# Optimization experiments

Hardware: AMD Instinct MI355X
Metric: run time of the kernel (lower is better)

Reference implementation:

```python
import jax, jax.numpy as jnp
import numpy as np

B, T, D, H = 64, 512, 512, 512

def setup_inputs() -> dict:
    key = jax.random.key(0)
    k1, k2, k3 = jax.random.split(key, 3)
    s_in = 1.0 / np.sqrt(D)
    s_h = 1.0 / np.sqrt(H)
    return {
        "x": jax.random.normal(k1, (B, T, D), dtype=jnp.float32),
        "Wi": jax.random.normal(k2, (D, 3 * H), dtype=jnp.float32) * s_in,  # packed [ir|iz|in]
        "bi": jnp.zeros((3 * H,), dtype=jnp.float32),
        "Wh": jax.random.normal(k3, (H, 3 * H), dtype=jnp.float32) * s_h,   # packed [hr|hz|hn]
        "bhn": jnp.zeros((H,), dtype=jnp.float32),
    }

def reference(x, Wi, bi, Wh, bhn):
    # Flax GRUCell semantics (sigmoid gates, tanh candidate), single layer,
    # zero initial carry, outputs stacked over time plus final carry.
    Bsz, Tlen, _ = x.shape
    Hdim = Wh.shape[0]
    # Precompute all input projections in one big GEMM: [B,T,3H]
    gi_all = jnp.einsum('btd,dk->btk', x, Wi) + bi

    def step(h, gi):
        hr, hz, hn = jnp.split(h @ Wh, 3, axis=-1)
        ir, iz, in_ = jnp.split(gi, 3, axis=-1)
        r = jax.nn.sigmoid(ir + hr)
        z = jax.nn.sigmoid(iz + hz)
        n = jnp.tanh(in_ + r * (hn + bhn))
        h_new = (1.0 - z) * n + z * h
        return h_new, h_new

    h0 = jnp.zeros((Bsz, Hdim), dtype=x.dtype)
    carry, ys = jax.lax.scan(step, h0, jnp.swapaxes(gi_all, 0, 1))  # scan over time
    outputs = jnp.swapaxes(ys, 0, 1)  # [B,T,H]
    return outputs, carry
```

## Files before the change

kernel.cpp:

```cpp
#include <hip/hip_runtime.h>


#define BSZ 64
#define TLEN 512
#define DDIM 512
#define HDIM 512
#define NGRP 4
#define PBLK 32
#define GB 16
#define SLOTB 16384
#define GRPB 65536
#define SENT32 0x40004000u
#define GUARD (1 << 16)

typedef _Float16 half8 __attribute__((ext_vector_type(8)));
typedef _Float16 half4v __attribute__((ext_vector_type(4)));
typedef float f32x4 __attribute__((ext_vector_type(4)));

__device__ __forceinline__ float sigmf(float v) { return 1.f / (1.f + __expf(-v)); }

__global__ void gru_setup(const float* __restrict__ x, _Float16* __restrict__ xb,
                          unsigned* __restrict__ exch) {
  size_t gid = (size_t)blockIdx.x * blockDim.x + threadIdx.x;
  size_t stride = (size_t)gridDim.x * blockDim.x;
  const float4* x4 = (const float4*)x;
  size_t nx4 = (size_t)BSZ * TLEN * DDIM / 4;
  for (size_t i = gid; i < nx4; i += stride) {
    float4 v = x4[i];
    half4v o = {(_Float16)v.x, (_Float16)v.y, (_Float16)v.z, (_Float16)v.w};
    *(half4v*)(xb + 4 * i) = o;
  }
  for (size_t i = gid; i < (size_t)NGRP * GRPB / 4; i += stride) exch[i] = SENT32;
}

__device__ __forceinline__ unsigned chk16(const half8* ah) {
  unsigned dirty = 0;
#pragma unroll
  for (int kt = 0; kt < 16; ++kt) {
    uint4 c;
    __builtin_memcpy(&c, &ah[kt], 16);
    unsigned bad = ((c.x & 0xFFFFu) == 0x4000u) | ((c.y & 0xFFFFu) == 0x4000u) |
                   ((c.z & 0xFFFFu) == 0x4000u) | ((c.w & 0xFFFFu) == 0x4000u);
    dirty |= bad << kt;
  }
  return dirty;
}

__global__ __launch_bounds__(192, 1) void gru_rec(
    const _Float16* __restrict__ xb, const float* __restrict__ Wi,
    const float* __restrict__ Wh, const float* __restrict__ bi,
    const float* __restrict__ bhn, char* __restrict__ exch,
    float* __restrict__ out) {
  __shared__ _Float16 Wh_l[48 * 512];
  __shared__ _Float16 Wi_l[48 * 512];
  __shared__ _Float16 Ah_l[16 * 512];
  __shared__ float Gh_l[2][3 * 256];
  __shared__ float Gx_l[2][3 * 256];

  const int tid = threadIdx.x;
  const int lane = tid & 63;
  const int wid = tid >> 6;
  const int g = blockIdx.x >> 5;
  const int rank = blockIdx.x & 31;
  const int c0 = rank * 16;
  char* const exg = exch + (size_t)g * GRPB;

  for (int idx = tid; idx < 48 * 512; idx += 192) {
    int k = idx / 48;
    int r = idx - k * 48;
    int gate = r >> 4, j = r & 15;
    int col = gate * 512 + c0 + j;
    int phys = (r << 10) | ((((k >> 3) << 4) ^ ((r & 7) << 4))) | ((k & 7) << 1);
    *(_Float16*)((char*)Wi_l + phys) = (_Float16)Wi[(size_t)k * 1536 + col];
    *(_Float16*)((char*)Wh_l + phys) = (_Float16)Wh[(size_t)k * 1536 + col];
  }

  const int m0 = lane >> 3;
  const int cp = (lane & 7) * 2;
  float bir[2], biz[2], bin_[2], bh2[2];
#pragma unroll
  for (int u = 0; u < 2; ++u) {
    bir[u] = bi[c0 + cp + u];
    biz[u] = bi[512 + c0 + cp + u];
    bin_[u] = bi[1024 + c0 + cp + u];
    bh2[u] = bhn[c0 + cp + u];
  }
  float hreg[2][2] = {{0.f, 0.f}, {0.f, 0.f}};
  __syncthreads();

  const int ar = lane & 15;
  const int kg = lane >> 4;
  const int wrow = wid * 16 + ar;
  const int mbat = g * GB + ar;
  const _Float16* const xrow = xb + (size_t)mbat * (TLEN * DDIM);
  char* const hbase = exg + ((kg >> 1) * 512 + ar * 32 + (kg & 1) * 16);
  const int abase = ar << 10;
  const int axor = (ar & 7) << 4;

  for (int t = 0; t < TLEN; ++t) {
    half8 a_x[16];
    const half8* xs = (const half8*)(xrow + (size_t)t * DDIM);
#pragma unroll
    for (int kt = 0; kt < 16; ++kt) a_x[kt] = xs[kt * 4 + kg];
    f32x4 acc_x = {0.f, 0.f, 0.f, 0.f};
#pragma unroll
    for (int kt = 0; kt < 16; ++kt) {
      const int off = (((kt * 4 + kg) << 4) ^ axor);
      half8 b_i = *(const half8*)((const char*)Wi_l + (wrow << 10) + off);
      acc_x = __builtin_amdgcn_mfma_f32_16x16x32_f16(a_x[kt], b_i, acc_x, 0, 0, 0);
    }

    if (wid == 2) {
      unsigned* rst = (unsigned*)(exg + ((t + 2) & 3) * SLOTB + rank * 512);
      __hip_atomic_store(rst + lane, SENT32, __ATOMIC_RELAXED, __HIP_MEMORY_SCOPE_AGENT);
      __hip_atomic_store(rst + 64 + lane, SENT32, __ATOMIC_RELAXED,
                         __HIP_MEMORY_SCOPE_AGENT);
    }
    if (wid == 1 && t > 0) {
      char* hb = hbase + (t & 3) * SLOTB;
      const char* p0 = hb;
      const char* p1 = hb + 4096;
      const char* p2 = hb + 8192;
      const char* p3 = hb + 12288;
      half8 ah[16];
      unsigned dirty;
      int guard = 0;
      do {
        asm volatile(
            "global_load_dwordx4 %0,  %16, off sc1\n\t"
            "global_load_dwordx4 %1,  %16, off offset:1024 sc1\n\t"
            "global_load_dwordx4 %2,  %16, off offset:2048 sc1\n\t"
            "global_load_dwordx4 %3,  %16, off offset:3072 sc1\n\t"
            "global_load_dwordx4 %4,  %17, off sc1\n\t"
            "global_load_dwordx4 %5,  %17, off offset:1024 sc1\n\t"
            "global_load_dwordx4 %6,  %17, off offset:2048 sc1\n\t"
            "global_load_dwordx4 %7,  %17, off offset:3072 sc1\n\t"
            "global_load_dwordx4 %8,  %18, off sc1\n\t"
            "global_load_dwordx4 %9,  %18, off offset:1024 sc1\n\t"
            "global_load_dwordx4 %10, %18, off offset:2048 sc1\n\t"
            "global_load_dwordx4 %11, %18, off offset:3072 sc1\n\t"
            "global_load_dwordx4 %12, %19, off sc1\n\t"
            "global_load_dwordx4 %13, %19, off offset:1024 sc1\n\t"
            "global_load_dwordx4 %14, %19, off offset:2048 sc1\n\t"
            "global_load_dwordx4 %15, %19, off offset:3072 sc1\n\t"
            "s_waitcnt vmcnt(0)"
            : "=&v"(ah[0]), "=&v"(ah[1]), "=&v"(ah[2]), "=&v"(ah[3]),
              "=&v"(ah[4]), "=&v"(ah[5]), "=&v"(ah[6]), "=&v"(ah[7]),
              "=&v"(ah[8]), "=&v"(ah[9]), "=&v"(ah[10]), "=&v"(ah[11]),
              "=&v"(ah[12]), "=&v"(ah[13]), "=&v"(ah[14]), "=&v"(ah[15])
            : "v"(p0), "v"(p1), "v"(p2), "v"(p3));
        dirty = chk16(ah);
      } while (__any(dirty != 0u) && ++guard < GUARD);
#pragma unroll
      for (int kt = 0; kt < 16; ++kt) {
        *(half8*)((char*)Ah_l + (abase | ((kt * 64 + kg * 16) ^ axor))) = ah[kt];
      }
    }
    __syncthreads();

    f32x4 acc_h = {0.f, 0.f, 0.f, 0.f};
    if (t > 0) {
#pragma unroll
      for (int kt = 0; kt < 16; ++kt) {
        half8 a_h = *(const half8*)((const char*)Ah_l +
                                    (abase | ((kt * 64 + kg * 16) ^ axor)));
        const int off = (((kt * 4 + kg) << 4) ^ axor);
        half8 b_h = *(const half8*)((const char*)Wh_l + (wrow << 10) + off);
        acc_h = __builtin_amdgcn_mfma_f32_16x16x32_f16(a_h, b_h, acc_h, 0, 0, 0);
      }
    }
#pragma unroll
    for (int q = 0; q < 4; ++q) {
      int row = kg * 4 + q;
      Gh_l[t & 1][wid * 256 + row * 16 + ar] = acc_h[q];
      Gx_l[t & 1][wid * 256 + row * 16 + ar] = acc_x[q];
    }
    __syncthreads();

    if (wid == 0) {
      const float* GhT = Gh_l[t & 1];
      const float* GxT = Gx_l[t & 1];
      char* pub = exg + ((t + 1) & 3) * SLOTB + rank * 512;
      float hn2[2][2];
#pragma unroll
      for (int bsel = 0; bsel < 2; ++bsel) {
        const int m = m0 + 8 * bsel;
#pragma unroll
        for (int u = 0; u < 2; ++u) {
          const int gi_ = m * 16 + cp + u;
          float r = sigmf(GxT[gi_] + GhT[gi_] + bir[u]);
          float z = sigmf(GxT[256 + gi_] + GhT[256 + gi_] + biz[u]);
          float pren = GxT[512 + gi_] + bin_[u] + r * (GhT[512 + gi_] + bh2[u]);
          float n = 2.f / (1.f + __expf(-2.f * pren)) - 1.f;
          hn2[bsel][u] = (1.f - z) * n + z * hreg[bsel][u];
          hreg[bsel][u] = hn2[bsel][u];
        }
        _Float16 q0 = (_Float16)hn2[bsel][0], q1 = (_Float16)hn2[bsel][1];
        unsigned pu = ((unsigned)*(unsigned short*)&q1 << 16) | *(unsigned short*)&q0;
        __hip_atomic_store((unsigned*)(pub + m * 32 + cp * 2), pu, __ATOMIC_RELAXED,
                           __HIP_MEMORY_SCOPE_AGENT);
      }
#pragma unroll
      for (int bsel = 0; bsel < 2; ++bsel) {
        const int b = g * GB + m0 + 8 * bsel;
        *(float2*)(out + ((size_t)b * TLEN + t) * HDIM + c0 + cp) =
            make_float2(hn2[bsel][0], hn2[bsel][1]);
      }
    }
  }

  if (wid == 0) {
#pragma unroll
    for (int bsel = 0; bsel < 2; ++bsel) {
      const int b = g * GB + m0 + 8 * bsel;
      *(float2*)(out + (size_t)BSZ * TLEN * HDIM + (size_t)b * HDIM + c0 + cp) =
          make_float2(hreg[bsel][0], hreg[bsel][1]);
    }
  }
}

extern "C" void kernel_launch(void* const* d_in, const int* in_sizes, int n_in,
                              void* d_out, int out_size, void* d_ws, size_t ws_size,
                              hipStream_t stream) {
  const float* x = (const float*)d_in[0];
  const float* Wi = (const float*)d_in[1];
  const float* bi = (const float*)d_in[2];
  const float* Wh = (const float*)d_in[3];
  const float* bhn = (const float*)d_in[4];
  float* out = (float*)d_out;

  char* ws = (char*)d_ws;
  _Float16* xb = (_Float16*)ws;
  char* exch = ws + 33554432;

  gru_setup<<<4096, 256, 0, stream>>>(x, xb, (unsigned*)exch);
  gru_rec<<<NGRP * PBLK, 192, 0, stream>>>(xb, Wi, Wh, bi, bhn, exch, out);
}
```

Measured before the change: 1.713 ms.

## Use row-major h exchange layout and issue h poll loads before input GEMM

Changes the global hidden-state exchange buffer to a batch-row-major layout, so each lane reads one contiguous 256-byte chunk instead of four strided pointers. The first poll of the recurrent state is issued at the top of the timestep, before the x-projection MFMAs, so its latency overlaps that compute; the spin loop only reloads when sentinel values remain. The publish and sentinel-reset addressing and the LDS store pattern are rewritten to match. This adds register pressure from holding the 16 prefetched vectors across the input GEMM.

```diff
diff --git a/kernel.cpp b/kernel.cpp
--- a/kernel.cpp
+++ b/kernel.cpp
@@ -11,6 +11,7 @@
 #define SLOTB 16384
 #define GRPB 65536
 #define SENT32 0x40004000u
+#define SENT64 0x4000400040004000ull
 #define GUARD (1 << 16)
 
 typedef _Float16 half8 __attribute__((ext_vector_type(8)));
@@ -93,11 +94,41 @@
   const int wrow = wid * 16 + ar;
   const int mbat = g * GB + ar;
   const _Float16* const xrow = xb + (size_t)mbat * (TLEN * DDIM);
-  char* const hbase = exg + ((kg >> 1) * 512 + ar * 32 + (kg & 1) * 16);
+  const int pb = lane >> 2;
+  const int pq = lane & 3;
+  const int sbase = pb << 10;
+  const int sxor = (pb & 7) << 4;
   const int abase = ar << 10;
   const int axor = (ar & 7) << 4;
 
   for (int t = 0; t < TLEN; ++t) {
+    half8 ah[16];
+    const char* pp = exg + (t & 3) * SLOTB + lane * 256;
+    if (wid == 1 && t > 0) {
+      asm volatile(
+          "global_load_dwordx4 %0,  %16, off sc1\n\t"
+          "global_load_dwordx4 %1,  %16, off offset:16 sc1\n\t"
+          "global_load_dwordx4 %2,  %16, off offset:32 sc1\n\t"
+          "global_load_dwordx4 %3,  %16, off offset:48 sc1\n\t"
+          "global_load_dwordx4 %4,  %16, off offset:64 sc1\n\t"
+          "global_load_dwordx4 %5,  %16, off offset:80 sc1\n\t"
+          "global_load_dwordx4 %6,  %16, off offset:96 sc1\n\t"
+          "global_load_dwordx4 %7,  %16, off offset:112 sc1\n\t"
+          "global_load_dwordx4 %8,  %16, off offset:128 sc1\n\t"
+          "global_load_dwordx4 %9,  %16, off offset:144 sc1\n\t"
+          "global_load_dwordx4 %10, %16, off offset:160 sc1\n\t"
+          "global_load_dwordx4 %11, %16, off offset:176 sc1\n\t"
+          "global_load_dwordx4 %12, %16, off offset:192 sc1\n\t"
+          "global_load_dwordx4 %13, %16, off offset:208 sc1\n\t"
+          "global_load_dwordx4 %14, %16, off offset:224 sc1\n\t"
+          "global_load_dwordx4 %15, %16, off offset:240 sc1"
+          : "=&v"(ah[0]), "=&v"(ah[1]), "=&v"(ah[2]), "=&v"(ah[3]),
+            "=&v"(ah[4]), "=&v"(ah[5]), "=&v"(ah[6]), "=&v"(ah[7]),
+            "=&v"(ah[8]), "=&v"(ah[9]), "=&v"(ah[10]), "=&v"(ah[11]),
+            "=&v"(ah[12]), "=&v"(ah[13]), "=&v"(ah[14]), "=&v"(ah[15])
+          : "v"(pp));
+    }
+
     half8 a_x[16];
     const half8* xs = (const half8*)(xrow + (size_t)t * DDIM);
 #pragma unroll
@@ -111,49 +142,46 @@
     }
 
     if (wid == 2) {
-      unsigned* rst = (unsigned*)(exg + ((t + 2) & 3) * SLOTB + rank * 512);
-      __hip_atomic_store(rst + lane, SENT32, __ATOMIC_RELAXED, __HIP_MEMORY_SCOPE_AGENT);
-      __hip_atomic_store(rst + 64 + lane, SENT32, __ATOMIC_RELAXED,
-                         __HIP_MEMORY_SCOPE_AGENT);
-    }
+      char* rst = exg + ((t + 2) & 3) * SLOTB;
+      __hip_atomic_store(
+          (unsigned long long*)(rst + pb * 1024 + c0 * 2 + pq * 8), SENT64,
+          __ATOMIC_RELAXED, __HIP_MEMORY_SCOPE_AGENT);
+    }
+
     if (wid == 1 && t > 0) {
-      char* hb = hbase + (t & 3) * SLOTB;
-      const char* p0 = hb;
-      const char* p1 = hb + 4096;
-      const char* p2 = hb + 8192;
-      const char* p3 = hb + 12288;
-      half8 ah[16];
-      unsigned dirty;
+      asm volatile("s_waitcnt vmcnt(0)" ::: "memory");
+      __builtin_amdgcn_sched_barrier(0);
+      unsigned dirty = chk16(ah);
       int guard = 0;
-      do {
+      while (__any(dirty != 0u) && ++guard < GUARD) {
         asm volatile(
             "global_load_dwordx4 %0,  %16, off sc1\n\t"
-            "global_load_dwordx4 %1,  %16, off offset:1024 sc1\n\t"
-            "global_load_dwordx4 %2,  %16, off offset:2048 sc1\n\t"
-            "global_load_dwordx4 %3,  %16, off offset:3072 sc1\n\t"
-            "global_load_dwordx4 %4,  %17, off sc1\n\t"
-            "global_load_dwordx4 %5,  %17, off offset:1024 sc1\n\t"
-            "global_load_dwordx4 %6,  %17, off offset:2048 sc1\n\t"
-            "global_load_dwordx4 %7,  %17, off offset:3072 sc1\n\t"
-            "global_load_dwordx4 %8,  %18, off sc1\n\t"
-            "global_load_dwordx4 %9,  %18, off offset:1024 sc1\n\t"
-            "global_load_dwordx4 %10, %18, off offset:2048 sc1\n\t"
-            "global_load_dwordx4 %11, %18, off offset:3072 sc1\n\t"
-            "global_load_dwordx4 %12, %19, off sc1\n\t"
-            "global_load_dwordx4 %13, %19, off offset:1024 sc1\n\t"
-            "global_load_dwordx4 %14, %19, off offset:2048 sc1\n\t"
-            "global_load_dwordx4 %15, %19, off offset:3072 sc1\n\t"
+            "global_load_dwordx4 %1,  %16, off offset:16 sc1\n\t"
+            "global_load_dwordx4 %2,  %16, off offset:32 sc1\n\t"
+            "global_load_dwordx4 %3,  %16, off offset:48 sc1\n\t"
+            "global_load_dwordx4 %4,  %16, off offset:64 sc1\n\t"
+            "global_load_dwordx4 %5,  %16, off offset:80 sc1\n\t"
+            "global_load_dwordx4 %6,  %16, off offset:96 sc1\n\t"
+            "global_load_dwordx4 %7,  %16, off offset:112 sc1\n\t"
+            "global_load_dwordx4 %8,  %16, off offset:128 sc1\n\t"
+            "global_load_dwordx4 %9,  %16, off offset:144 sc1\n\t"
+            "global_load_dwordx4 %10, %16, off offset:160 sc1\n\t"
+            "global_load_dwordx4 %11, %16, off offset:176 sc1\n\t"
+            "global_load_dwordx4 %12, %16, off offset:192 sc1\n\t"
+            "global_load_dwordx4 %13, %16, off offset:208 sc1\n\t"
+            "global_load_dwordx4 %14, %16, off offset:224 sc1\n\t"
+            "global_load_dwordx4 %15, %16, off offset:240 sc1\n\t"
             "s_waitcnt vmcnt(0)"
             : "=&v"(ah[0]), "=&v"(ah[1]), "=&v"(ah[2]), "=&v"(ah[3]),
               "=&v"(ah[4]), "=&v"(ah[5]), "=&v"(ah[6]), "=&v"(ah[7]),
               "=&v"(ah[8]), "=&v"(ah[9]), "=&v"(ah[10]), "=&v"(ah[11]),
               "=&v"(ah[12]), "=&v"(ah[13]), "=&v"(ah[14]), "=&v"(ah[15])
-            : "v"(p0), "v"(p1), "v"(p2), "v"(p3));
+            : "v"(pp));
         dirty = chk16(ah);
-      } while (__any(dirty != 0u) && ++guard < GUARD);
-#pragma unroll
-      for (int kt = 0; kt < 16; ++kt) {
-        *(half8*)((char*)Ah_l + (abase | ((kt * 64 + kg * 16) ^ axor))) = ah[kt];
+      }
+#pragma unroll
+      for (int c = 0; c < 16; ++c) {
+        *(half8*)((char*)Ah_l + (sbase | ((pq * 256 + c * 16) ^ sxor))) = ah[c];
       }
     }
     __syncthreads();
@@ -180,7 +208,7 @@
     if (wid == 0) {
       const float* GhT = Gh_l[t & 1];
       const float* GxT = Gx_l[t & 1];
-      char* pub = exg + ((t + 1) & 3) * SLOTB + rank * 512;
+      char* pub = exg + ((t + 1) & 3) * SLOTB;
       float hn2[2][2];
 #pragma unroll
       for (int bsel = 0; bsel < 2; ++bsel) {
@@ -197,8 +225,8 @@
         }
         _Float16 q0 = (_Float16)hn2[bsel][0], q1 = (_Float16)hn2[bsel][1];
         unsigned pu = ((unsigned)*(unsigned short*)&q1 << 16) | *(unsigned short*)&q0;
-        __hip_atomic_store((unsigned*)(pub + m * 32 + cp * 2), pu, __ATOMIC_RELAXED,
-                           __HIP_MEMORY_SCOPE_AGENT);
+        __hip_atomic_store((unsigned*)(pub + m * 1024 + (c0 + cp) * 2), pu,
+                           __ATOMIC_RELAXED, __HIP_MEMORY_SCOPE_AGENT);
       }
 #pragma unroll
       for (int bsel = 0; bsel < 2; ++bsel) {
```

Result: slower. 3.009 ms (+75.6%).

## Hoist input projection into separate parallel GEMM and halve recurrent block count

Applied to the files above, without the earlier changes.

Adds a standalone MFMA GEMM kernel that computes all input projections plus bias into an fp16 workspace before the recurrence, instead of computing x·Wi inside every timestep of the serial loop. The recurrent kernel now uses 16 blocks per group with 32 columns each and 6 waves, so only the h·Wh product stays on the critical path and fewer blocks take part in each step's exchange. This removes per-step x loads and Wi MFMAs from the latency-bound loop, at the cost of a large fp16 gi buffer (about 100MB) and extra memory traffic. It falls back to the old path if the workspace is too small.

```diff
diff --git a/kernel.cpp b/kernel.cpp
--- a/kernel.cpp
+++ b/kernel.cpp
@@ -5,12 +5,8 @@
 #define TLEN 512
 #define DDIM 512
 #define HDIM 512
-#define NGRP 4
-#define PBLK 32
-#define GB 16
-#define SLOTB 16384
-#define GRPB 65536
 #define SENT32 0x40004000u
+#define SENT64 0x4000400040004000ull
 #define GUARD (1 << 16)
 
 typedef _Float16 half8 __attribute__((ext_vector_type(8)));
@@ -18,6 +14,257 @@
 typedef float f32x4 __attribute__((ext_vector_type(4)));
 
 __device__ __forceinline__ float sigmf(float v) { return 1.f / (1.f + __expf(-v)); }
+__device__ __forceinline__ float lo16(unsigned u) {
+  unsigned short s = (unsigned short)(u & 0xffffu);
+  _Float16 f;
+  __builtin_memcpy(&f, &s, 2);
+  return (float)f;
+}
+__device__ __forceinline__ float hi16(unsigned u) {
+  unsigned short s = (unsigned short)(u >> 16);
+  _Float16 f;
+  __builtin_memcpy(&f, &s, 2);
+  return (float)f;
+}
+
+__device__ __forceinline__ unsigned chk16(const half8* ah) {
+  unsigned dirty = 0;
+#pragma unroll
+  for (int kt = 0; kt < 16; ++kt) {
+    uint4 c;
+    __builtin_memcpy(&c, &ah[kt], 16);
+    unsigned bad = ((c.x & 0xFFFFu) == 0x4000u) | ((c.y & 0xFFFFu) == 0x4000u) |
+                   ((c.z & 0xFFFFu) == 0x4000u) | ((c.w & 0xFFFFu) == 0x4000u);
+    dirty |= bad << kt;
+  }
+  return dirty;
+}
+
+#define SWEEP16(AH, P0, P1, P2, P3)                                           \
+  asm volatile(                                                               \
+      "global_load_dwordx4 %0,  %16, off sc1\n\t"                             \
+      "global_load_dwordx4 %1,  %16, off offset:1024 sc1\n\t"                 \
+      "global_load_dwordx4 %2,  %16, off offset:2048 sc1\n\t"                 \
+      "global_load_dwordx4 %3,  %16, off offset:3072 sc1\n\t"                 \
+      "global_load_dwordx4 %4,  %17, off sc1\n\t"                             \
+      "global_load_dwordx4 %5,  %17, off offset:1024 sc1\n\t"                 \
+      "global_load_dwordx4 %6,  %17, off offset:2048 sc1\n\t"                 \
+      "global_load_dwordx4 %7,  %17, off offset:3072 sc1\n\t"                 \
+      "global_load_dwordx4 %8,  %18, off sc1\n\t"                             \
+      "global_load_dwordx4 %9,  %18, off offset:1024 sc1\n\t"                 \
+      "global_load_dwordx4 %10, %18, off offset:2048 sc1\n\t"                 \
+      "global_load_dwordx4 %11, %18, off offset:3072 sc1\n\t"                 \
+      "global_load_dwordx4 %12, %19, off sc1\n\t"                             \
+      "global_load_dwordx4 %13, %19, off offset:1024 sc1\n\t"                 \
+      "global_load_dwordx4 %14, %19, off offset:2048 sc1\n\t"                 \
+      "global_load_dwordx4 %15, %19, off offset:3072 sc1\n\t"                 \
+      "s_waitcnt vmcnt(0)"                                                    \
+      : "=&v"(AH[0]), "=&v"(AH[1]), "=&v"(AH[2]), "=&v"(AH[3]), "=&v"(AH[4]), \
+        "=&v"(AH[5]), "=&v"(AH[6]), "=&v"(AH[7]), "=&v"(AH[8]), "=&v"(AH[9]), \
+        "=&v"(AH[10]), "=&v"(AH[11]), "=&v"(AH[12]), "=&v"(AH[13]),           \
+        "=&v"(AH[14]), "=&v"(AH[15])                                          \
+      : "v"(P0), "v"(P1), "v"(P2), "v"(P3))
+
+
+__global__ void setup_fast(unsigned* __restrict__ exch) {
+  size_t gid = (size_t)blockIdx.x * blockDim.x + threadIdx.x;
+  size_t stride = (size_t)gridDim.x * blockDim.x;
+  for (size_t i = gid; i < 65536; i += stride) exch[i] = SENT32;
+}
+
+__global__ __launch_bounds__(384, 1) void gemm_gi(const float* __restrict__ x,
+                                                  const float* __restrict__ Wi,
+                                                  const float* __restrict__ bi,
+                                                  _Float16* __restrict__ gi) {
+  __shared__ _Float16 W_l[96 * 512];
+  __shared__ _Float16 A_l[16 * 512];
+  __shared__ _Float16 O_l[16 * 96];
+
+  const int tid = threadIdx.x;
+  const int lane = tid & 63;
+  const int wid = tid >> 6;
+  const int cb = blockIdx.x & 15;
+  const int mp = blockIdx.x >> 4;
+  const int n0 = cb * 96;
+
+  for (int idx = tid; idx < 96 * 512; idx += 384) {
+    int k = idx / 96;
+    int r = idx - k * 96;
+    int phys = (r << 10) | ((((k >> 3) << 4) ^ ((r & 7) << 4))) | ((k & 7) << 1);
+    *(_Float16*)((char*)W_l + phys) = (_Float16)Wi[(size_t)k * 1536 + n0 + r];
+  }
+  const int ar = lane & 15;
+  const int kg = lane >> 4;
+  const int wrow = wid * 16 + ar;
+  const int axor = (ar & 7) << 4;
+  const float bin = bi[n0 + wid * 16 + ar];
+  __syncthreads();
+
+  const float4* x4 = (const float4*)x;
+  for (int mc = 0; mc < 64; ++mc) {
+    const int m0 = (mp * 64 + mc) * 16;
+    for (int i = tid; i < 2048; i += 384) {
+      int r = i >> 7, kq = i & 127, k = kq * 4;
+      float4 v = x4[(size_t)(m0 + r) * 128 + kq];
+      half4v o = {(_Float16)v.x, (_Float16)v.y, (_Float16)v.z, (_Float16)v.w};
+      int phys = (r << 10) | ((((k >> 3) << 4) ^ ((r & 7) << 4))) | ((k & 7) << 1);
+      *(half4v*)((char*)A_l + phys) = o;
+    }
+    __syncthreads();
+    f32x4 acc = {0.f, 0.f, 0.f, 0.f};
+#pragma unroll
+    for (int kt = 0; kt < 16; ++kt) {
+      const int off = (((kt * 4 + kg) << 4) ^ axor);
+      half8 a = *(const half8*)((const char*)A_l + (ar << 10) + off);
+      half8 b = *(const half8*)((const char*)W_l + (wrow << 10) + off);
+      acc = __builtin_amdgcn_mfma_f32_16x16x32_f16(a, b, acc, 0, 0, 0);
+    }
+#pragma unroll
+    for (int q = 0; q < 4; ++q)
+      O_l[(kg * 4 + q) * 96 + wid * 16 + ar] = (_Float16)(acc[q] + bin);
+    __syncthreads();
+    {
+      int row = tid / 24, seg = tid % 24;
+      if (row < 16) {
+        *(unsigned long long*)(gi + (size_t)(m0 + row) * 1536 + n0 + seg * 4) =
+            ((const unsigned long long*)O_l)[row * 24 + seg];
+      }
+    }
+    __syncthreads();
+  }
+}
+
+__global__ __launch_bounds__(384, 1) void gru_rec16(
+    const _Float16* __restrict__ gi, const float* __restrict__ Wh,
+    const float* __restrict__ bhn, char* __restrict__ exch,
+    float* __restrict__ out) {
+  __shared__ _Float16 Wh_l[96 * 512];
+  __shared__ _Float16 Ah_l[16 * 512];
+  __shared__ float Gh_l[2][6 * 256];
+
+  const int tid = threadIdx.x;
+  const int lane = tid & 63;
+  const int wid = tid >> 6;
+  const int g = blockIdx.x >> 4;
+  const int rank = blockIdx.x & 15;
+  const int c0 = rank * 32;
+  char* const exg = exch + (size_t)g * 65536;
+
+  for (int idx = tid; idx < 96 * 512; idx += 384) {
+    int k = idx / 96;
+    int r = idx - k * 96;
+    int col = (r >> 5) * 512 + c0 + (r & 31);
+    int phys = (r << 10) | ((((k >> 3) << 4) ^ ((r & 7) << 4))) | ((k & 7) << 1);
+    *(_Float16*)((char*)Wh_l + phys) = (_Float16)Wh[(size_t)k * 1536 + col];
+  }
+
+  const int e0 = ((wid & 3) * 64 + lane) * 2;
+  const int m = e0 >> 5;
+  const int c = e0 & 31;
+  const int bglob = g * 16 + m;
+  const _Float16* const giR =
+      gi + (size_t)bglob * TLEN * 1536 + c0 + c;
+  const _Float16* const giZ = giR + 512;
+  const _Float16* const giN = giR + 1024;
+  float bh2[2];
+  bh2[0] = bhn[c0 + c];
+  bh2[1] = bhn[c0 + c + 1];
+  float hreg[2] = {0.f, 0.f};
+  __syncthreads();
+
+  const int ar = lane & 15;
+  const int kg = lane >> 4;
+  const int wrow = wid * 16 + ar;
+  const int axor = (ar & 7) << 4;
+  const int abase = ar << 10;
+  char* const hbase = exg + ar * 64 + kg * 16;
+
+  for (int t = 0; t < TLEN; ++t) {
+    if (wid == 4) {
+      unsigned long long* rst = (unsigned long long*)(exg + ((t + 2) & 3) * 16384 +
+                                                      rank * 1024 + lane * 16);
+      __hip_atomic_store(rst, SENT64, __ATOMIC_RELAXED, __HIP_MEMORY_SCOPE_AGENT);
+      __hip_atomic_store(rst + 1, SENT64, __ATOMIC_RELAXED, __HIP_MEMORY_SCOPE_AGENT);
+    }
+    unsigned ur = 0, uz = 0, un = 0;
+    if (wid < 4) {
+      const size_t toff = (size_t)t * 1536;
+      ur = *(const unsigned*)(giR + toff);
+      uz = *(const unsigned*)(giZ + toff);
+      un = *(const unsigned*)(giN + toff);
+    }
+    if (wid == 5 && t > 0) {
+      char* hb = hbase + (t & 3) * 16384;
+      const char* p0 = hb;
+      const char* p1 = hb + 4096;
+      const char* p2 = hb + 8192;
+      const char* p3 = hb + 12288;
+      half8 ah[16];
+      unsigned dirty;
+      int guard = 0;
+      do {
+        SWEEP16(ah, p0, p1, p2, p3);
+        dirty = chk16(ah);
+      } while (__any(dirty != 0u) && ++guard < GUARD);
+#pragma unroll
+      for (int kt = 0; kt < 16; ++kt) {
+        *(half8*)((char*)Ah_l + (abase | ((kt * 64 + kg * 16) ^ axor))) = ah[kt];
+      }
+    }
+    __syncthreads();
+
+    f32x4 acc_h = {0.f, 0.f, 0.f, 0.f};
+    if (t > 0) {
+#pragma unroll
+      for (int kt = 0; kt < 16; ++kt) {
+        half8 a_h = *(const half8*)((const char*)Ah_l +
+                                    (abase | ((kt * 64 + kg * 16) ^ axor)));
+        const int off = (((kt * 4 + kg) << 4) ^ axor);
+        half8 b_h = *(const half8*)((const char*)Wh_l + (wrow << 10) + off);
+        acc_h = __builtin_amdgcn_mfma_f32_16x16x32_f16(a_h, b_h, acc_h, 0, 0, 0);
+      }
+    }
+#pragma unroll
+    for (int q = 0; q < 4; ++q)
+      Gh_l[t & 1][wid * 256 + (kg * 4 + q) * 16 + ar] = acc_h[q];
+    __syncthreads();
+
+    if (wid < 4) {
+      const float* GhT = Gh_l[t & 1];
+      const int ti = (c >> 4);
+      const int cc = c & 15;
+      float hn2[2];
+      const float gir[2] = {lo16(ur), hi16(ur)};
+      const float giz[2] = {lo16(uz), hi16(uz)};
+      const float gin[2] = {lo16(un), hi16(un)};
+#pragma unroll
+      for (int u = 0; u < 2; ++u) {
+        const int gidx = m * 16 + cc + u;
+        float hr = GhT[(0 * 2 + ti) * 256 + gidx];
+        float hz = GhT[(1 * 2 + ti) * 256 + gidx];
+        float hn = GhT[(2 * 2 + ti) * 256 + gidx];
+        float r = sigmf(gir[u] + hr);
+        float z = sigmf(giz[u] + hz);
+        float pren = gin[u] + r * (hn + bh2[u]);
+        float n = 2.f / (1.f + __expf(-2.f * pren)) - 1.f;
+        hn2[u] = (1.f - z) * n + z * hreg[u];
+        hreg[u] = hn2[u];
+      }
+      _Float16 q0 = (_Float16)hn2[0], q1 = (_Float16)hn2[1];
+      unsigned pu = ((unsigned)*(unsigned short*)&q1 << 16) | *(unsigned short*)&q0;
+      __hip_atomic_store(
+          (unsigned*)(exg + ((t + 1) & 3) * 16384 + rank * 1024 + m * 64 + c * 2),
+          pu, __ATOMIC_RELAXED, __HIP_MEMORY_SCOPE_AGENT);
+      *(float2*)(out + ((size_t)bglob * TLEN + t) * HDIM + c0 + c) =
+          make_float2(hn2[0], hn2[1]);
+    }
+  }
+  if (wid < 4) {
+    *(float2*)(out + (size_t)BSZ * TLEN * HDIM + (size_t)bglob * HDIM + c0 + c) =
+        make_float2(hreg[0], hreg[1]);
+  }
+}
+
 
 __global__ void gru_setup(const float* __restrict__ x, _Float16* __restrict__ xb,
                           unsigned* __restrict__ exch) {
@@ -30,20 +277,7 @@
     half4v o = {(_Float16)v.x, (_Float16)v.y, (_Float16)v.z, (_Float16)v.w};
     *(half4v*)(xb + 4 * i) = o;
   }
-  for (size_t i = gid; i < (size_t)NGRP * GRPB / 4; i += stride) exch[i] = SENT32;
-}
-
-__device__ __forceinline__ unsigned chk16(const half8* ah) {
-  unsigned dirty = 0;
-#pragma unroll
-  for (int kt = 0; kt < 16; ++kt) {
-    uint4 c;
-    __builtin_memcpy(&c, &ah[kt], 16);
-    unsigned bad = ((c.x & 0xFFFFu) == 0x4000u) | ((c.y & 0xFFFFu) == 0x4000u) |
-                   ((c.z & 0xFFFFu) == 0x4000u) | ((c.w & 0xFFFFu) == 0x4000u);
-    dirty |= bad << kt;
-  }
-  return dirty;
+  for (size_t i = gid; i < 65536; i += stride) exch[i] = SENT32;
 }
 
 __global__ __launch_bounds__(192, 1) void gru_rec(
@@ -63,7 +297,7 @@
   const int g = blockIdx.x >> 5;
   const int rank = blockIdx.x & 31;
   const int c0 = rank * 16;
-  char* const exg = exch + (size_t)g * GRPB;
+  char* const exg = exch + (size_t)g * 65536;
 
   for (int idx = tid; idx < 48 * 512; idx += 192) {
     int k = idx / 48;
@@ -74,7 +308,6 @@
     *(_Float16*)((char*)Wi_l + phys) = (_Float16)Wi[(size_t)k * 1536 + col];
     *(_Float16*)((char*)Wh_l + phys) = (_Float16)Wh[(size_t)k * 1536 + col];
   }
-
   const int m0 = lane >> 3;
   const int cp = (lane & 7) * 2;
   float bir[2], biz[2], bin_[2], bh2[2];
@@ -91,13 +324,18 @@
   const int ar = lane & 15;
   const int kg = lane >> 4;
   const int wrow = wid * 16 + ar;
-  const int mbat = g * GB + ar;
-  const _Float16* const xrow = xb + (size_t)mbat * (TLEN * DDIM);
+  const int axor = (ar & 7) << 4;
+  const int abase = ar << 10;
+  const _Float16* const xrow = xb + (size_t)(g * 16 + ar) * (TLEN * DDIM);
   char* const hbase = exg + ((kg >> 1) * 512 + ar * 32 + (kg & 1) * 16);
-  const int abase = ar << 10;
-  const int axor = (ar & 7) << 4;
 
   for (int t = 0; t < TLEN; ++t) {
+    if (wid == 2) {
+      unsigned* rst = (unsigned*)(exg + ((t + 2) & 3) * 16384 + rank * 512);
+      __hip_atomic_store(rst + lane, SENT32, __ATOMIC_RELAXED, __HIP_MEMORY_SCOPE_AGENT);
+      __hip_atomic_store(rst + 64 + lane, SENT32, __ATOMIC_RELAXED,
+                         __HIP_MEMORY_SCOPE_AGENT);
+    }
     half8 a_x[16];
     const half8* xs = (const half8*)(xrow + (size_t)t * DDIM);
 #pragma unroll
@@ -109,15 +347,8 @@
       half8 b_i = *(const half8*)((const char*)Wi_l + (wrow << 10) + off);
       acc_x = __builtin_amdgcn_mfma_f32_16x16x32_f16(a_x[kt], b_i, acc_x, 0, 0, 0);
     }
-
-    if (wid == 2) {
-      unsigned* rst = (unsigned*)(exg + ((t + 2) & 3) * SLOTB + rank * 512);
-      __hip_atomic_store(rst + lane, SENT32, __ATOMIC_RELAXED, __HIP_MEMORY_SCOPE_AGENT);
-      __hip_atomic_store(rst + 64 + lane, SENT32, __ATOMIC_RELAXED,
-                         __HIP_MEMORY_SCOPE_AGENT);
-    }
     if (wid == 1 && t > 0) {
-      char* hb = hbase + (t & 3) * SLOTB;
+      char* hb = hbase + (t & 3) * 16384;
       const char* p0 = hb;
       const char* p1 = hb + 4096;
       const char* p2 = hb + 8192;
@@ -126,38 +357,14 @@
       unsigned dirty;
       int guard = 0;
       do {
-        asm volatile(
-            "global_load_dwordx4 %0,  %16, off sc1\n\t"
-            "global_load_dwordx4 %1,  %16, off offset:1024 sc1\n\t"
-            "global_load_dwordx4 %2,  %16, off offset:2048 sc1\n\t"
-            "global_load_dwordx4 %3,  %16, off offset:3072 sc1\n\t"
-            "global_load_dwordx4 %4,  %17, off sc1\n\t"
-            "global_load_dwordx4 %5,  %17, off offset:1024 sc1\n\t"
-            "global_load_dwordx4 %6,  %17, off offset:2048 sc1\n\t"
-            "global_load_dwordx4 %7,  %17, off offset:3072 sc1\n\t"
-            "global_load_dwordx4 %8,  %18, off sc1\n\t"
-            "global_load_dwordx4 %9,  %18, off offset:1024 sc1\n\t"
-            "global_load_dwordx4 %10, %18, off offset:2048 sc1\n\t"
-            "global_load_dwordx4 %11, %18, off offset:3072 sc1\n\t"
-            "global_load_dwordx4 %12, %19, off sc1\n\t"
-            "global_load_dwordx4 %13, %19, off offset:1024 sc1\n\t"
-            "global_load_dwordx4 %14, %19, off offset:2048 sc1\n\t"
-            "global_load_dwordx4 %15, %19, off offset:3072 sc1\n\t"
-            "s_waitcnt vmcnt(0)"
-            : "=&v"(ah[0]), "=&v"(ah[1]), "=&v"(ah[2]), "=&v"(ah[3]),
-              "=&v"(ah[4]), "=&v"(ah[5]), "=&v"(ah[6]), "=&v"(ah[7]),
-              "=&v"(ah[8]), "=&v"(ah[9]), "=&v"(ah[10]), "=&v"(ah[11]),
-              "=&v"(ah[12]), "=&v"(ah[13]), "=&v"(ah[14]), "=&v"(ah[15])
-            : "v"(p0), "v"(p1), "v"(p2), "v"(p3));
+        SWEEP16(ah, p0, p1, p2, p3);
         dirty = chk16(ah);
       } while (__any(dirty != 0u) && ++guard < GUARD);
 #pragma unroll
-      for (int kt = 0; kt < 16; ++kt) {
+      for (int kt = 0; kt < 16; ++kt)
         *(half8*)((char*)Ah_l + (abase | ((kt * 64 + kg * 16) ^ axor))) = ah[kt];
-      }
-    }
-    __syncthreads();
-
+    }
+    __syncthreads();
     f32x4 acc_h = {0.f, 0.f, 0.f, 0.f};
     if (t > 0) {
 #pragma unroll
@@ -176,18 +383,17 @@
       Gx_l[t & 1][wid * 256 + row * 16 + ar] = acc_x[q];
     }
     __syncthreads();
-
     if (wid == 0) {
       const float* GhT = Gh_l[t & 1];
       const float* GxT = Gx_l[t & 1];
-      char* pub = exg + ((t + 1) & 3) * SLOTB + rank * 512;
+      char* pub = exg + ((t + 1) & 3) * 16384 + rank * 512;
       float hn2[2][2];
 #pragma unroll
       for (int bsel = 0; bsel < 2; ++bsel) {
-        const int m = m0 + 8 * bsel;
+        const int mm = m0 + 8 * bsel;
 #pragma unroll
         for (int u = 0; u < 2; ++u) {
-          const int gi_ = m * 16 + cp + u;
+          const int gi_ = mm * 16 + cp + u;
           float r = sigmf(GxT[gi_] + GhT[gi_] + bir[u]);
           float z = sigmf(GxT[256 + gi_] + GhT[256 + gi_] + biz[u]);
           float pren = GxT[512 + gi_] + bin_[u] + r * (GhT[512 + gi_] + bh2[u]);
@@ -197,27 +403,27 @@
         }
         _Float16 q0 = (_Float16)hn2[bsel][0], q1 = (_Float16)hn2[bsel][1];
         unsigned pu = ((unsigned)*(unsigned short*)&q1 << 16) | *(unsigned short*)&q0;
-        __hip_atomic_store((unsigned*)(pub + m * 32 + cp * 2), pu, __ATOMIC_RELAXED,
+        __hip_atomic_store((unsigned*)(pub + mm * 32 + cp * 2), pu, __ATOMIC_RELAXED,
                            __HIP_MEMORY_SCOPE_AGENT);
       }
 #pragma unroll
       for (int bsel = 0; bsel < 2; ++bsel) {
-        const int b = g * GB + m0 + 8 * bsel;
+        const int b = g * 16 + m0 + 8 * bsel;
         *(float2*)(out + ((size_t)b * TLEN + t) * HDIM + c0 + cp) =
             make_float2(hn2[bsel][0], hn2[bsel][1]);
       }
     }
   }
-
   if (wid == 0) {
 #pragma unroll
     for (int bsel = 0; bsel < 2; ++bsel) {
-      const int b = g * GB + m0 + 8 * bsel;
+      const int b = g * 16 + m0 + 8 * bsel;
       *(float2*)(out + (size_t)BSZ * TLEN * HDIM + (size_t)b * HDIM + c0 + cp) =
           make_float2(hreg[bsel][0], hreg[bsel][1]);
     }
   }
 }
+
 
 extern "C" void kernel_launch(void* const* d_in, const int* in_sizes, int n_in,
                               void* d_out, int out_size, void* d_ws, size_t ws_size,
@@ -228,11 +434,21 @@
   const float* Wh = (const float*)d_in[3];
   const float* bhn = (const float*)d_in[4];
   float* out = (float*)d_out;
-
   char* ws = (char*)d_ws;
-  _Float16* xb = (_Float16*)ws;
-  char* exch = ws + 33554432;
-
-  gru_setup<<<4096, 256, 0, stream>>>(x, xb, (unsigned*)exch);
-  gru_rec<<<NGRP * PBLK, 192, 0, stream>>>(xb, Wi, Wh, bi, bhn, exch, out);
-}
+
+  const size_t GI_BYTES = (size_t)BSZ * TLEN * 1536 * 2;
+  const size_t NEED = GI_BYTES + 262144;
+
+  if (ws_size >= NEED) {
+    _Float16* gi = (_Float16*)ws;
+    char* exch = ws + GI_BYTES;
+    setup_fast<<<256, 256, 0, stream>>>((unsigned*)exch);
+    gemm_gi<<<512, 384, 0, stream>>>(x, Wi, bi, gi);
+    gru_rec16<<<64, 384, 0, stream>>>(gi, Wh, bhn, exch, out);
+  } else {
+    _Float16* xb = (_Float16*)ws;
+    char* exch = ws + 33554432;
+    gru_setup<<<4096, 256, 0, stream>>>(x, xb, (unsigned*)exch);
+    gru_rec<<<4 * 32, 192, 0, stream>>>(xb, Wi, Wh, bi, bhn, exch, out);
+  }
+}
```

Measured after the change: 2.117 ms. 23.6% more time.
